# Kernel optimization log

Measured on AMD Instinct MI355X. Metric: run time of the kernel, lower is better.

The kernel has to match this reference:

```python
import math
import jax, jax.numpy as jnp
import numpy as np

H, C, PQ, PV = 8, 256, 8, 12   # no_heads, c_hidden, no_qk_points, no_v_points
INF, EPS = 1e5, 1e-8

def quat_to_rot(q):
    w, x, y, z = q[..., 0], q[..., 1], q[..., 2], q[..., 3]
    r = jnp.stack([
        1 - 2*(y*y + z*z), 2*(x*y - w*z),     2*(x*z + w*y),
        2*(x*y + w*z),     1 - 2*(x*x + z*z), 2*(y*z - w*x),
        2*(x*z - w*y),     2*(y*z + w*x),     1 - 2*(x*x + y*y),
    ], axis=-1)
    return r.reshape(q.shape[:-1] + (3, 3))

def setup_inputs() -> dict:
    key = jax.random.key(0)
    ks = jax.random.split(key, 16)
    B, N, CS, CZ = 1, 512, 384, 128
    s = jax.random.normal(ks[0], (B, N, CS), jnp.float32)
    z = jax.random.normal(ks[1], (B, N, N, CZ), jnp.float32) * 0.1
    quat = jax.random.normal(ks[2], (B, N, 4), jnp.float32)
    quat = quat / jnp.linalg.norm(quat, axis=-1, keepdims=True)
    rot = quat_to_rot(quat)                       # [B,N,3,3] valid rotations
    trans = jax.random.normal(ks[3], (B, N, 3), jnp.float32) * 10.0
    mask = jnp.ones((B, N), jnp.float32)
    g = lambda k, sh: jax.random.normal(k, sh, jnp.float32) * 0.02
    params = dict(
        wq=g(ks[4], (CS, H*C)), bq=jnp.zeros((H*C,), jnp.float32),
        wkv=g(ks[5], (CS, 2*H*C)), bkv=jnp.zeros((2*H*C,), jnp.float32),
        wqp=g(ks[6], (CS, H*PQ*3)), bqp=jnp.zeros((H*PQ*3,), jnp.float32),
        wkvp=g(ks[7], (CS, H*(PQ+PV)*3)), bkvp=jnp.zeros((H*(PQ+PV)*3,), jnp.float32),
        wb=g(ks[8], (CZ, H)), bb=jnp.zeros((H,), jnp.float32),
        wz=g(ks[9], (CZ, CZ//4)), bz=jnp.zeros((CZ//4,), jnp.float32),
        head_weights=jnp.full((H,), 0.541324854612918, jnp.float32),  # softplus^-1(1)
        wo=g(ks[10], (H*(C + 4*PV + CZ//4), CS)), bo=jnp.zeros((CS,), jnp.float32),
    )
    return dict(s=s, z=z, rot=rot, trans=trans, mask=mask, **params)

def reference(s, z, rot, trans, mask, wq, bq, wkv, bkv, wqp, bqp, wkvp, bkvp, wb, bb, wz, bz, head_weights, wo, bo):
    B, N, CS = s.shape
    q = (s @ wq + bq).reshape(B, N, H, C)
    kv = (s @ wkv + bkv).reshape(B, N, H, 2 * C)
    k, v = kv[..., :C], kv[..., C:]

    def split_pts(x):  # torch split-into-3 + stack(-1): [B,N,3*M] -> [B,N,M,3]
        return jnp.moveaxis(x.reshape(B, N, 3, -1), -2, -1)

    def apply_rigid(p):  # global frame: R @ p + t
        return jnp.einsum('bnij,bnpj->bnpi', rot, p) + trans[:, :, None, :]

    q_pts = apply_rigid(split_pts(s @ wqp + bqp)).reshape(B, N, H, PQ, 3)
    kv_pts = apply_rigid(split_pts(s @ wkvp + bkvp)).reshape(B, N, H, PQ + PV, 3)
    k_pts, v_pts = kv_pts[..., :PQ, :], kv_pts[..., PQ:, :]

    b_bias = z @ wb + bb                                  # [B,Ni,Nj,H]
    a = jnp.einsum('bihc,bjhc->bhij', q, k) * math.sqrt(1.0 / (3 * C))
    a = a + math.sqrt(1.0 / 3) * jnp.moveaxis(b_bias, -1, 1)

    disp = q_pts[:, :, None] - k_pts[:, None]             # [B,Ni,Nj,H,PQ,3]
    pt_att = jnp.sum(disp * disp, axis=-1)                # [B,Ni,Nj,H,PQ]
    hw = jax.nn.softplus(head_weights) * math.sqrt(1.0 / (3 * (PQ * 9.0 / 2)))
    pt_att = -0.5 * jnp.sum(pt_att * hw[None, None, None, :, None], axis=-1)  # [B,Ni,Nj,H]

    sq_mask = INF * (mask[:, :, None] * mask[:, None, :] - 1.0)
    a = a + jnp.moveaxis(pt_att, -1, 1) + sq_mask[:, None]
    a = jax.nn.softmax(a, axis=-1)                        # [B,H,Ni,Nj]

    o = jnp.einsum('bhij,bjhc->bihc', a, v).reshape(B, N, H * C)

    o_pt = jnp.einsum('bhij,bjhpd->bihpd', a, v_pts)      # [B,N,H,PV,3] global
    o_pt = jnp.einsum('bnji,bnhpj->bnhpi', rot, o_pt - trans[:, :, None, None, :])  # invert_apply
    o_pt_norm = jnp.sqrt(jnp.sum(o_pt * o_pt, axis=-1) + EPS).reshape(B, N, H * PV)
    o_pt_flat = o_pt.reshape(B, N, H * PV, 3)

    pair_z = z @ wz + bz                                  # [B,Ni,Nj,CZ//4]
    o_pair = jnp.einsum('bhij,bijd->bihd', a, pair_z).reshape(B, N, -1)

    feats = jnp.concatenate(
        [o, o_pt_flat[..., 0], o_pt_flat[..., 1], o_pt_flat[..., 2], o_pt_norm, o_pair], axis=-1)
    return feats @ wo + bo
```

## Files before the change

kernel.cpp:

```cpp
#include <hip/hip_runtime.h>


#define OFF_QBH    0
#define OFF_KBH    524288
#define OFF_VB     1048576
#define OFF_QPRAW  2097152
#define OFF_KVPRAW 2195456
#define OFF_BBIAS  2785280
#define OFF_PAIRZT 3833856
#define OFF_ATTNH  8028160
#define OFF_FEATSB 9076736
#define OFF_WCAT   9764864
#define OFF_WTALL  9767936
#define OFF_VPT    11082752
#define OFF_WOT    11803648
#define OFF_QPTH   12319744
#define OFF_QPTL   12385280
#define OFF_KPTH   12450816
#define OFF_KPTL   12516352
#define OFF_QP2    12581888
#define OFF_KP2    12585984
#define OFF_SBF    12590080

typedef __attribute__((ext_vector_type(8))) short short8;
typedef __attribute__((ext_vector_type(4))) float f32x4;

__device__ __forceinline__ unsigned short f2bf(float f) {
  union { float f; unsigned u; } v; v.f = f;
  unsigned u = v.u;
  unsigned r = (u + 0x7fffu + ((u >> 16) & 1u)) >> 16;
  return (unsigned short)r;
}
__device__ __forceinline__ float bf2f(unsigned short h) {
  union { unsigned u; float f; } v; v.u = ((unsigned)h) << 16; return v.f;
}
__device__ __forceinline__ short8 pack8(float4 a, float4 b) {
  short8 r;
  r[0] = (short)f2bf(a.x); r[1] = (short)f2bf(a.y);
  r[2] = (short)f2bf(a.z); r[3] = (short)f2bf(a.w);
  r[4] = (short)f2bf(b.x); r[5] = (short)f2bf(b.y);
  r[6] = (short)f2bf(b.z); r[7] = (short)f2bf(b.w);
  return r;
}

__global__ __launch_bounds__(256) void prep_all(
    const float* __restrict__ wq, const float* __restrict__ wkv,
    const float* __restrict__ wqp, const float* __restrict__ wkvp,
    const float* __restrict__ wo, const float* __restrict__ wb,
    const float* __restrict__ wz, const float* __restrict__ s,
    unsigned short* __restrict__ wTall, unsigned short* __restrict__ woT,
    unsigned short* __restrict__ wT, unsigned short* __restrict__ sbf) {
  __shared__ float tile[64][65];
  const int b = blockIdx.x, t = threadIdx.x;
  if (b < 642) {
    const int ntile = b % 107, kt = b / 107;
    const float* src; int Nsrc, nloc0;
    const int ng0 = ntile * 64;
    if (ntile < 32)      { src = wq;   Nsrc = 2048; nloc0 = ng0; }
    else if (ntile < 96) { src = wkv;  Nsrc = 4096; nloc0 = ng0 - 2048; }
    else if (ntile < 99) { src = wqp;  Nsrc = 192;  nloc0 = ng0 - 6144; }
    else                 { src = wkvp; Nsrc = 480;  nloc0 = ng0 - 6336; }
    const int r = t >> 2, cs = (t & 3) * 16;
#pragma unroll
    for (int i = 0; i < 16; i += 4) {
      int n = nloc0 + cs + i;
      float4 v;
      if (n + 3 < Nsrc) v = *(const float4*)(src + (size_t)(kt * 64 + r) * Nsrc + n);
      else {
        v.x = (n + 0 < Nsrc) ? src[(size_t)(kt * 64 + r) * Nsrc + n + 0] : 0.f;
        v.y = (n + 1 < Nsrc) ? src[(size_t)(kt * 64 + r) * Nsrc + n + 1] : 0.f;
        v.z = (n + 2 < Nsrc) ? src[(size_t)(kt * 64 + r) * Nsrc + n + 2] : 0.f;
        v.w = (n + 3 < Nsrc) ? src[(size_t)(kt * 64 + r) * Nsrc + n + 3] : 0.f;
      }
      tile[r][cs + i + 0] = v.x; tile[r][cs + i + 1] = v.y;
      tile[r][cs + i + 2] = v.z; tile[r][cs + i + 3] = v.w;
    }
    __syncthreads();
    const int nr = t >> 2, ks = (t & 3) * 16;
    unsigned short ov[16];
#pragma unroll
    for (int i = 0; i < 16; i++) ov[i] = f2bf(tile[ks + i][nr]);
    unsigned short* dst = wTall + (size_t)(ng0 + nr) * 384 + kt * 64 + ks;
    *(uint4*)(dst) = *(const uint4*)&ov[0];
    *(uint4*)(dst + 8) = *(const uint4*)&ov[8];
  } else if (b < 894) {
    const int idx = b - 642;
    const int kt = idx % 42, ntile = idx / 42;
    const int r = t >> 2, cs = (t & 3) * 16;
#pragma unroll
    for (int i = 0; i < 16; i += 4) {
      float4 v = *(const float4*)(wo + (size_t)(kt * 64 + r) * 384 + ntile * 64 + cs + i);
      tile[r][cs + i + 0] = v.x; tile[r][cs + i + 1] = v.y;
      tile[r][cs + i + 2] = v.z; tile[r][cs + i + 3] = v.w;
    }
    __syncthreads();
    const int nr = t >> 2, ks = (t & 3) * 16;
    unsigned short ov[16];
#pragma unroll
    for (int i = 0; i < 16; i++) ov[i] = f2bf(tile[ks + i][nr]);
    unsigned short* dst = woT + (size_t)(ntile * 64 + nr) * 2688 + kt * 64 + ks;
    *(uint4*)(dst) = *(const uint4*)&ov[0];
    *(uint4*)(dst + 8) = *(const uint4*)&ov[8];
  } else if (b < 918) {
    const int l = (b - 894) * 256 + t;
    if (l < 6144) {
      int n = l >> 7, k = l & 127;
      float v = (n < 8) ? wb[k * 8 + n] * 0.5773502691896258f
                        : (n < 40 ? wz[k * 32 + (n - 8)] : 0.f);
      wT[l] = f2bf(v);
    }
  } else {
    const int gid = (b - 918) * 256 + t;
    const int off = gid * 8;
    float4 a0 = *(const float4*)(s + off);
    float4 a1 = *(const float4*)(s + off + 4);
    *(short8*)(sbf + off) = pack8(a0, a1);
  }
}

__global__ __launch_bounds__(256) void mega1(
    const float* __restrict__ z, const unsigned short* __restrict__ wT,
    const float* __restrict__ bb, const float* __restrict__ bz,
    unsigned short* __restrict__ bbias_tb, unsigned short* __restrict__ pairzT,
    const unsigned short* __restrict__ sbf, const unsigned short* __restrict__ wTall,
    const float* __restrict__ bq, const float* __restrict__ bkv,
    const float* __restrict__ bqp, const float* __restrict__ bkvp,
    unsigned short* __restrict__ qbh, unsigned short* __restrict__ kbh,
    float* __restrict__ vb, float* __restrict__ qpraw, float* __restrict__ kvpraw) {
  __shared__ __align__(16) unsigned short lb[4][8][16];
  __shared__ __align__(16) unsigned short lp[4][32][16];
  const int lane = threadIdx.x & 63, wv = threadIdx.x >> 6;
  const int quad = lane >> 4, m = lane & 15;
  if (blockIdx.x < 4096) {
    const int tile = blockIdx.x * 4 + wv;
    const int row0 = tile * 16;
    short8 bf[3][4];
#pragma unroll
    for (int nt = 0; nt < 3; nt++)
#pragma unroll
      for (int s = 0; s < 4; s++)
        bf[nt][s] = *(const short8*)(wT + (size_t)(nt * 16 + m) * 128 + s * 32 + quad * 8);
    float bias[3];
#pragma unroll
    for (int nt = 0; nt < 3; nt++) {
      int c = nt * 16 + m;
      bias[nt] = (c < 8) ? 0.5773502691896258f * bb[c] : (c < 40 ? bz[c - 8] : 0.f);
    }
    f32x4 acc[3];
#pragma unroll
    for (int nt = 0; nt < 3; nt++) acc[nt] = (f32x4){0.f, 0.f, 0.f, 0.f};
    const float* zr = z + (size_t)(row0 + m) * 128 + quad * 8;
#pragma unroll
    for (int s = 0; s < 4; s++) {
      float4 a0 = *(const float4*)(zr + s * 32);
      float4 a1 = *(const float4*)(zr + s * 32 + 4);
      short8 af = pack8(a0, a1);
#pragma unroll
      for (int nt = 0; nt < 3; nt++)
        acc[nt] = __builtin_amdgcn_mfma_f32_16x16x32_bf16(af, bf[nt][s], acc[nt], 0, 0, 0);
    }
#pragma unroll
    for (int nt = 0; nt < 3; nt++) {
      const int c = nt * 16 + m;
#pragma unroll
      for (int r = 0; r < 4; r++) {
        const float v = acc[nt][r] + bias[nt];
        const int jl = quad * 4 + r;
        if (c < 8)       lb[wv][c][jl] = f2bf(v);
        else if (c < 40) lp[wv][c - 8][jl] = f2bf(v);
      }
    }
    const int i = row0 >> 9, j0 = row0 & 511;
    if (lane < 16) {
      int c = lane >> 1, half = lane & 1;
      uint4 val = *(const uint4*)&lb[wv][c][half * 8];
      *(uint4*)(bbias_tb + (size_t)c * 262144 + row0 + half * 8) = val;
    }
    {
      int d = lane >> 1, half = lane & 1;
      uint4 val = *(const uint4*)&lp[wv][d][half * 8];
      *(uint4*)(pairzT + ((size_t)i * 32 + d) * 512 + j0 + half * 8) = val;
    }
  } else {
    const int b2 = blockIdx.x - 4096;
    const int bx = b2 % 107, row0 = (b2 / 107) * 64;
    const int n0 = bx * 64;
    const unsigned short* srow = sbf + (size_t)(row0 + wv * 16 + m) * 384;
    f32x4 acc[4];
#pragma unroll
    for (int nt = 0; nt < 4; nt++) acc[nt] = (f32x4){0.f, 0.f, 0.f, 0.f};
#pragma unroll
    for (int ksx = 0; ksx < 12; ksx++) {
      const int c0 = ksx * 32 + quad * 8;
      short8 af = *(const short8*)(srow + c0);
#pragma unroll
      for (int nt = 0; nt < 4; nt++) {
        short8 bfw = *(const short8*)(wTall + (size_t)(n0 + nt * 16 + m) * 384 + c0);
        acc[nt] = __builtin_amdgcn_mfma_f32_16x16x32_bf16(af, bfw, acc[nt], 0, 0, 0);
      }
    }
    const int rbase = row0 + wv * 16 + quad * 4;
#pragma unroll
    for (int nt = 0; nt < 4; nt++) {
      const int col = n0 + nt * 16 + m;
      if (n0 < 2048) {
        const float bias = bq[col];
#pragma unroll
        for (int r = 0; r < 4; r++)
          qbh[(size_t)(rbase + r) * 2048 + col] = f2bf(acc[nt][r] + bias);
      } else if (n0 < 6144) {
        const int ckv = col - 2048;
        const float bias = bkv[ckv];
        const int hh = ckv >> 9, c = ckv & 511;
        if (c < 256) {
#pragma unroll
          for (int r = 0; r < 4; r++)
            kbh[(size_t)(rbase + r) * 2048 + hh * 256 + c] = f2bf(acc[nt][r] + bias);
        } else {
#pragma unroll
          for (int r = 0; r < 4; r++)
            vb[(size_t)(rbase + r) * 2048 + hh * 256 + (c - 256)] = acc[nt][r] + bias;
        }
      } else if (n0 < 6336) {
        const int cq = col - 6144;
        const float bias = bqp[cq];
#pragma unroll
        for (int r = 0; r < 4; r++)
          qpraw[(size_t)(rbase + r) * 192 + cq] = acc[nt][r] + bias;
      } else {
        const int ck = col - 6336;
        if (ck < 480) {
          const float bias = bkvp[ck];
#pragma unroll
          for (int r = 0; r < 4; r++)
            kvpraw[(size_t)(rbase + r) * 480 + ck] = acc[nt][r] + bias;
        }
      }
    }
  }
}

__global__ __launch_bounds__(256) void mega2(
    const float* __restrict__ vb, const float* __restrict__ qpraw,
    const float* __restrict__ kvpraw, const float* __restrict__ rot,
    const float* __restrict__ trans, unsigned short* __restrict__ vptT,
    unsigned short* __restrict__ qptH, unsigned short* __restrict__ qptL,
    unsigned short* __restrict__ kptH, unsigned short* __restrict__ kptL,
    float* __restrict__ qp2g, float* __restrict__ kp2g) {
  __shared__ float tile[64][65];
  const int b = blockIdx.x, t = threadIdx.x;
  if (b < 320) {
    const int jt = b & 7, h = (b >> 3) & 7, part = b >> 6;
    const int j0 = jt * 64;
    if (part < 4) {
      const int c0 = part * 64;
      const int r = t >> 2, cs = (t & 3) * 16;
#pragma unroll
      for (int ii = 0; ii < 16; ii += 4) {
        float4 v = *(const float4*)(vb + (size_t)(j0 + r) * 2048 + h * 256 + c0 + cs + ii);
        tile[r][cs + ii + 0] = v.x; tile[r][cs + ii + 1] = v.y;
        tile[r][cs + ii + 2] = v.z; tile[r][cs + ii + 3] = v.w;
      }
      __syncthreads();
      const int cl = t >> 2, js = (t & 3) * 16;
      unsigned short ov[16];
#pragma unroll
      for (int x = 0; x < 16; x++) ov[x] = f2bf(tile[js + x][cl]);
      unsigned short* dst = vptT + ((size_t)h * 352 + c0 + cl) * 512 + j0 + js;
      *(uint4*)dst = *(const uint4*)&ov[0];
      *(uint4*)(dst + 8) = *(const uint4*)&ov[8];
    } else {
      float (*lds)[37] = (float(*)[37])&tile[0][0];
      for (int l = t; l < 64 * 36; l += 256) {
        int jl = l / 36, w = l % 36;
        int p = w / 3, d = w % 3;
        const int n = j0 + jl;
        const int pidx = h * 20 + 8 + p;
        const float* kr = kvpraw + (size_t)n * 480;
        float px = kr[pidx], py = kr[160 + pidx], pz = kr[320 + pidx];
        const float* R = rot + n * 9;
        lds[jl][w] = R[d * 3 + 0] * px + R[d * 3 + 1] * py + R[d * 3 + 2] * pz + trans[n * 3 + d];
      }
      __syncthreads();
#pragma unroll
      for (int step = 0; step < 3; step++) {
        int chunk = t + 256 * step;
        int row = chunk >> 3, js = (chunk & 7) * 8;
        unsigned short ov[8];
#pragma unroll
        for (int x = 0; x < 8; x++) {
          int w = (row < 48) ? row : row - 48;
          float f = (w < 36) ? lds[js + x][w] : 0.f;
          unsigned short hi = f2bf(f);
          ov[x] = (row < 48) ? hi : f2bf(f - bf2f(hi));
        }
        *(uint4*)(vptT + ((size_t)h * 352 + 256 + row) * 512 + j0 + js) = *(const uint4*)&ov[0];
      }
    }
  } else {
    const int idx = b - 320;
    const int row = (idx & 1) * 256 + t;
    const int h = idx >> 1;
    const float* R  = rot + row * 9;
    const float* tr = trans + row * 3;
    {
      const float* qr = qpraw + (size_t)row * 192;
      unsigned short hi[32], lo[32]; float s2 = 0.f;
#pragma unroll
      for (int p = 0; p < 8; p++) {
        const int pidx = h * 8 + p;
        float px = qr[pidx], py = qr[64 + pidx], pz = qr[128 + pidx];
        float X = R[0] * px + R[1] * py + R[2] * pz + tr[0];
        float Y = R[3] * px + R[4] * py + R[5] * pz + tr[1];
        float Z = R[6] * px + R[7] * py + R[8] * pz + tr[2];
        hi[p * 3 + 0] = f2bf(X); lo[p * 3 + 0] = f2bf(X - bf2f(hi[p * 3 + 0]));
        hi[p * 3 + 1] = f2bf(Y); lo[p * 3 + 1] = f2bf(Y - bf2f(hi[p * 3 + 1]));
        hi[p * 3 + 2] = f2bf(Z); lo[p * 3 + 2] = f2bf(Z - bf2f(hi[p * 3 + 2]));
        s2 += X * X + Y * Y + Z * Z;
      }
#pragma unroll
      for (int w = 24; w < 32; w++) { hi[w] = 0; lo[w] = 0; }
      unsigned short* dh = qptH + ((size_t)h * 512 + row) * 32;
      unsigned short* dl = qptL + ((size_t)h * 512 + row) * 32;
#pragma unroll
      for (int g = 0; g < 4; g++) {
        *(uint4*)(dh + g * 8) = *(const uint4*)&hi[g * 8];
        *(uint4*)(dl + g * 8) = *(const uint4*)&lo[g * 8];
      }
      qp2g[h * 512 + row] = s2;
    }
    {
      const float* kr = kvpraw + (size_t)row * 480;
      unsigned short hi[32], lo[32]; float s2 = 0.f;
#pragma unroll
      for (int p = 0; p < 8; p++) {
        const int pidx = h * 20 + p;
        float px = kr[pidx], py = kr[160 + pidx], pz = kr[320 + pidx];
        float X = R[0] * px + R[1] * py + R[2] * pz + tr[0];
        float Y = R[3] * px + R[4] * py + R[5] * pz + tr[1];
        float Z = R[6] * px + R[7] * py + R[8] * pz + tr[2];
        hi[p * 3 + 0] = f2bf(X); lo[p * 3 + 0] = f2bf(X - bf2f(hi[p * 3 + 0]));
        hi[p * 3 + 1] = f2bf(Y); lo[p * 3 + 1] = f2bf(Y - bf2f(hi[p * 3 + 1]));
        hi[p * 3 + 2] = f2bf(Z); lo[p * 3 + 2] = f2bf(Z - bf2f(hi[p * 3 + 2]));
        s2 += X * X + Y * Y + Z * Z;
      }
#pragma unroll
      for (int w = 24; w < 32; w++) { hi[w] = 0; lo[w] = 0; }
      unsigned short* dh = kptH + ((size_t)h * 512 + row) * 32;
      unsigned short* dl = kptL + ((size_t)h * 512 + row) * 32;
#pragma unroll
      for (int g = 0; g < 4; g++) {
        *(uint4*)(dh + g * 8) = *(const uint4*)&hi[g * 8];
        *(uint4*)(dl + g * 8) = *(const uint4*)&lo[g * 8];
      }
      kp2g[h * 512 + row] = s2;
    }
  }
}

__global__ __launch_bounds__(512) void logits_fused(
    const unsigned short* __restrict__ qbh, const unsigned short* __restrict__ kbh,
    const unsigned short* __restrict__ qptH, const unsigned short* __restrict__ qptL,
    const unsigned short* __restrict__ kptH, const unsigned short* __restrict__ kptL,
    const float* __restrict__ qp2g, const float* __restrict__ kp2g,
    const unsigned short* __restrict__ bbias_tb, const float* __restrict__ mask,
    const float* __restrict__ hwp, const unsigned short* __restrict__ vptT,
    const float* __restrict__ rot, const float* __restrict__ trans,
    unsigned short* __restrict__ attnh, unsigned short* __restrict__ featsb) {
  const int it = blockIdx.x, h = blockIdx.y;
  const int i0 = it * 16;
  __shared__ __align__(16) unsigned short sth[8][16][72], stl[8][16][72];
  __shared__ float redm[16][8], reds[16][8];
  __shared__ float lds_h[16][48], lds_l[16][48];
  const int t = threadIdx.x;
  const int lane = t & 63, wv = t >> 6;
  const int quad = lane >> 4, m = lane & 15;
  const int jw0 = wv * 64;

  f32x4 acc[4];
#pragma unroll
  for (int nt = 0; nt < 4; nt++) acc[nt] = (f32x4){0.f, 0.f, 0.f, 0.f};
  const unsigned short* qrow = qbh + (size_t)(i0 + m) * 2048 + h * 256;
#pragma unroll
  for (int s = 0; s < 8; s++) {
    short8 af = *(const short8*)(qrow + s * 32 + quad * 8);
#pragma unroll
    for (int nt = 0; nt < 4; nt++) {
      short8 bfr = *(const short8*)(kbh + (size_t)(jw0 + nt * 16 + m) * 2048 + h * 256 + s * 32 + quad * 8);
      acc[nt] = __builtin_amdgcn_mfma_f32_16x16x32_bf16(af, bfr, acc[nt], 0, 0, 0);
    }
  }

  short8 aqh = *(const short8*)(qptH + ((size_t)h * 512 + i0 + m) * 32 + quad * 8);
  short8 aql = *(const short8*)(qptL + ((size_t)h * 512 + i0 + m) * 32 + quad * 8);
  f32x4 accp[4];
#pragma unroll
  for (int nt = 0; nt < 4; nt++) {
    const size_t krow = ((size_t)h * 512 + jw0 + nt * 16 + m) * 32 + quad * 8;
    short8 bkh = *(const short8*)(kptH + krow);
    short8 bkl = *(const short8*)(kptL + krow);
    f32x4 p = (f32x4){0.f, 0.f, 0.f, 0.f};
    p = __builtin_amdgcn_mfma_f32_16x16x32_bf16(aqh, bkh, p, 0, 0, 0);
    p = __builtin_amdgcn_mfma_f32_16x16x32_bf16(aqh, bkl, p, 0, 0, 0);
    p = __builtin_amdgcn_mfma_f32_16x16x32_bf16(aql, bkh, p, 0, 0, 0);
    accp[nt] = p;
  }

  const float c1 = 0.03608439182435161f;
  const float hw = log1pf(expf(hwp[h])) * 0.09622504486493764f;
  float qp2v[4];
#pragma unroll
  for (int r = 0; r < 4; r++) qp2v[r] = qp2g[h * 512 + i0 + quad * 4 + r];
  float lg[4][4];
  float rmax[4] = {-1e30f, -1e30f, -1e30f, -1e30f};
#pragma unroll
  for (int nt = 0; nt < 4; nt++) {
    const int j = jw0 + nt * 16 + m;
    const float kp2v = kp2g[h * 512 + j];
    const float mj = mask[j];
#pragma unroll
    for (int r = 0; r < 4; r++) {
      const int il = quad * 4 + r;
      const float pt = qp2v[r] + kp2v - 2.f * accp[nt][r];
      float v = c1 * acc[nt][r]
              + bf2f(bbias_tb[(size_t)h * 262144 + (size_t)(i0 + il) * 512 + j])
              - 0.5f * hw * pt
              + 100000.f * (mask[i0 + il] * mj - 1.f);
      lg[nt][r] = v;
      rmax[r] = fmaxf(rmax[r], v);
    }
  }
#pragma unroll
  for (int r = 0; r < 4; r++) {
#pragma unroll
    for (int off = 1; off < 16; off <<= 1) rmax[r] = fmaxf(rmax[r], __shfl_xor(rmax[r], off));
  }
  if (m == 0) {
#pragma unroll
    for (int r = 0; r < 4; r++) redm[quad * 4 + r][wv] = rmax[r];
  }
  __syncthreads();
  float rowm[4], rsum[4];
#pragma unroll
  for (int r = 0; r < 4; r++) {
    const int il = quad * 4 + r;
    float m0 = fmaxf(fmaxf(redm[il][0], redm[il][1]), fmaxf(redm[il][2], redm[il][3]));
    float m1 = fmaxf(fmaxf(redm[il][4], redm[il][5]), fmaxf(redm[il][6], redm[il][7]));
    rowm[r] = fmaxf(m0, m1);
    rsum[r] = 0.f;
  }
#pragma unroll
  for (int nt = 0; nt < 4; nt++)
#pragma unroll
    for (int r = 0; r < 4; r++) {
      float e = __expf(lg[nt][r] - rowm[r]);
      lg[nt][r] = e;
      rsum[r] += e;
    }
#pragma unroll
  for (int r = 0; r < 4; r++) {
#pragma unroll
    for (int off = 1; off < 16; off <<= 1) rsum[r] += __shfl_xor(rsum[r], off);
  }
  if (m == 0) {
#pragma unroll
    for (int r = 0; r < 4; r++) reds[quad * 4 + r][wv] = rsum[r];
  }
  __syncthreads();
  float inv[4];
#pragma unroll
  for (int r = 0; r < 4; r++) {
    const int il = quad * 4 + r;
    float s0 = (reds[il][0] + reds[il][1]) + (reds[il][2] + reds[il][3]);
    float s1 = (reds[il][4] + reds[il][5]) + (reds[il][6] + reds[il][7]);
    inv[r] = 1.f / (s0 + s1);
  }
#pragma unroll
  for (int nt = 0; nt < 4; nt++)
#pragma unroll
    for (int r = 0; r < 4; r++) {
      const int il = quad * 4 + r;
      float a = lg[nt][r] * inv[r];
      unsigned short hi = f2bf(a);
      sth[wv][il][nt * 16 + m] = hi;
      stl[wv][il][nt * 16 + m] = f2bf(a - bf2f(hi));
    }
  __syncthreads();
#pragma unroll
  for (int step = 0; step < 2; step++) {
    const int idx = lane + 64 * step;
    const int il = idx >> 3, seg = idx & 7;
    uint4 vh = *(const uint4*)&sth[wv][il][seg * 8];
    *(uint4*)(attnh + ((size_t)h * 512 + i0 + il) * 512 + jw0 + seg * 8) = vh;
  }

  const int nt0 = (wv < 6) ? wv * 3 : 18 + (wv - 6) * 2;
  const int ncnt = (wv < 6) ? 3 : 2;
  f32x4 vacc[3];
#pragma unroll
  for (int k = 0; k < 3; k++) vacc[k] = (f32x4){0.f, 0.f, 0.f, 0.f};
  const unsigned short* vbase = vptT + (size_t)h * 352 * 512;
#pragma unroll
  for (int s = 0; s < 16; s++) {
    const int wsrc = s >> 1, col = (s & 1) * 32 + quad * 8;
    short8 ah = *(const short8*)&sth[wsrc][m][col];
    short8 al = *(const short8*)&stl[wsrc][m][col];
    const int ko = s * 32 + quad * 8;
#pragma unroll
    for (int k = 0; k < 3; k++) {
      if (k < ncnt) {
        const int nt = nt0 + k;
        short8 bfr = *(const short8*)(vbase + (size_t)(nt * 16 + m) * 512 + ko);
        vacc[k] = __builtin_amdgcn_mfma_f32_16x16x32_bf16(ah, bfr, vacc[k], 0, 0, 0);
        if (nt >= 16 && nt < 19)
          vacc[k] = __builtin_amdgcn_mfma_f32_16x16x32_bf16(al, bfr, vacc[k], 0, 0, 0);
      }
    }
  }
#pragma unroll
  for (int k = 0; k < 3; k++) {
    if (k < ncnt) {
      const int nt = nt0 + k;
      if (nt < 16) {
#pragma unroll
        for (int r = 0; r < 4; r++)
          featsb[(size_t)(i0 + quad * 4 + r) * 2688 + h * 256 + nt * 16 + m] = f2bf(vacc[k][r]);
      } else if (nt < 19) {
        const int w = (nt - 16) * 16 + m;
#pragma unroll
        for (int r = 0; r < 4; r++) if (w < 36) lds_h[quad * 4 + r][w] = vacc[k][r];
      } else {
        const int w = (nt - 19) * 16 + m;
#pragma unroll
        for (int r = 0; r < 4; r++) if (w < 36) lds_l[quad * 4 + r][w] = vacc[k][r];
      }
    }
  }
  __syncthreads();
  if (t < 192) {
    const int il = t / 12, p = t % 12, irow = i0 + il;
    const float* R = rot + irow * 9;
    const float* tr = trans + irow * 3;
    float x  = lds_h[il][p * 3 + 0] + lds_l[il][p * 3 + 0] - tr[0];
    float y  = lds_h[il][p * 3 + 1] + lds_l[il][p * 3 + 1] - tr[1];
    float zz = lds_h[il][p * 3 + 2] + lds_l[il][p * 3 + 2] - tr[2];
    float o0 = R[0] * x + R[3] * y + R[6] * zz;
    float o1 = R[1] * x + R[4] * y + R[7] * zz;
    float o2 = R[2] * x + R[5] * y + R[8] * zz;
    float nrm = sqrtf(o0 * o0 + o1 * o1 + o2 * o2 + 1e-8f);
    unsigned short* fr = featsb + (size_t)irow * 2688 + 2048;
    fr[h * 12 + p]       = f2bf(o0);
    fr[96 + h * 12 + p]  = f2bf(o1);
    fr[192 + h * 12 + p] = f2bf(o2);
    fr[288 + h * 12 + p] = f2bf(nrm);
  }
}

__global__ __launch_bounds__(256) void o_pair_mfma(
    const unsigned short* __restrict__ attnh, const unsigned short* __restrict__ pairzT,
    unsigned short* __restrict__ featsb) {
  const int lane = threadIdx.x & 63, wv = threadIdx.x >> 6;
  const int quad = lane >> 4, m = lane & 15;
  const int i = blockIdx.x * 4 + wv;
  f32x4 acc[2];
  acc[0] = (f32x4){0.f, 0.f, 0.f, 0.f};
  acc[1] = (f32x4){0.f, 0.f, 0.f, 0.f};
#pragma unroll
  for (int s = 0; s < 16; s++) {
    const int ko = s * 32 + quad * 8;
    short8 af = *(const short8*)(attnh + (size_t)(m & 7) * 262144 + (size_t)i * 512 + ko);
#pragma unroll
    for (int nt = 0; nt < 2; nt++) {
      short8 bfr = *(const short8*)(pairzT + ((size_t)i * 32 + nt * 16 + m) * 512 + ko);
      acc[nt] = __builtin_amdgcn_mfma_f32_16x16x32_bf16(af, bfr, acc[nt], 0, 0, 0);
    }
  }
  if (quad < 2) {
#pragma unroll
    for (int nt = 0; nt < 2; nt++)
#pragma unroll
      for (int r = 0; r < 4; r++) {
        const int hh = quad * 4 + r, d = nt * 16 + m;
        featsb[(size_t)i * 2688 + 2432 + hh * 32 + d] = f2bf(acc[nt][r]);
      }
  }
}

__global__ __launch_bounds__(256) void out_mfma(
    const unsigned short* __restrict__ featsb, const unsigned short* __restrict__ woT,
    const float* __restrict__ bo, float* __restrict__ out) {
  const int it = blockIdx.x, ng = blockIdx.y;
  const int lane = threadIdx.x & 63, wv = threadIdx.x >> 6;
  const int quad = lane >> 4, m = lane & 15;
  const int i0 = it * 16, n0 = (ng * 4 + wv) * 16;
  const unsigned short* arow = featsb + (size_t)(i0 + m) * 2688;
  const unsigned short* brow = woT + (size_t)(n0 + m) * 2688;
  f32x4 acc = (f32x4){0.f, 0.f, 0.f, 0.f};
#pragma unroll 4
  for (int s = 0; s < 84; s++) {
    const int ko = s * 32 + quad * 8;
    short8 af = *(const short8*)(arow + ko);
    short8 bf = *(const short8*)(brow + ko);
    acc = __builtin_amdgcn_mfma_f32_16x16x32_bf16(af, bf, acc, 0, 0, 0);
  }
  const float bias = bo[n0 + m];
#pragma unroll
  for (int r = 0; r < 4; r++)
    out[(size_t)(i0 + quad * 4 + r) * 384 + n0 + m] = acc[r] + bias;
}

extern "C" void kernel_launch(void* const* d_in, const int* in_sizes, int n_in,
                              void* d_out, int out_size, void* d_ws, size_t ws_size,
                              hipStream_t stream) {
  const float* s     = (const float*)d_in[0];
  const float* z     = (const float*)d_in[1];
  const float* rot   = (const float*)d_in[2];
  const float* trans = (const float*)d_in[3];
  const float* mask  = (const float*)d_in[4];
  const float* wq    = (const float*)d_in[5];
  const float* bq    = (const float*)d_in[6];
  const float* wkv   = (const float*)d_in[7];
  const float* bkv   = (const float*)d_in[8];
  const float* wqp   = (const float*)d_in[9];
  const float* bqp   = (const float*)d_in[10];
  const float* wkvp  = (const float*)d_in[11];
  const float* bkvp  = (const float*)d_in[12];
  const float* wb    = (const float*)d_in[13];
  const float* bb    = (const float*)d_in[14];
  const float* wz    = (const float*)d_in[15];
  const float* bz    = (const float*)d_in[16];
  const float* hwp   = (const float*)d_in[17];
  const float* wo    = (const float*)d_in[18];
  const float* bo    = (const float*)d_in[19];
  float* out = (float*)d_out;

  float* ws = (float*)d_ws;
  unsigned short* qbh   = (unsigned short*)(ws + OFF_QBH);
  unsigned short* kbh   = (unsigned short*)(ws + OFF_KBH);
  float* vb      = ws + OFF_VB;
  float* qpraw   = ws + OFF_QPRAW;
  float* kvpraw  = ws + OFF_KVPRAW;
  unsigned short* bbias_tb = (unsigned short*)(ws + OFF_BBIAS);
  unsigned short* pairzT   = (unsigned short*)(ws + OFF_PAIRZT);
  unsigned short* attnh    = (unsigned short*)(ws + OFF_ATTNH);
  unsigned short* featsb   = (unsigned short*)(ws + OFF_FEATSB);
  unsigned short* wT    = (unsigned short*)(ws + OFF_WCAT);
  unsigned short* wTall = (unsigned short*)(ws + OFF_WTALL);
  unsigned short* vptT  = (unsigned short*)(ws + OFF_VPT);
  unsigned short* woT   = (unsigned short*)(ws + OFF_WOT);
  unsigned short* qptH  = (unsigned short*)(ws + OFF_QPTH);
  unsigned short* qptL  = (unsigned short*)(ws + OFF_QPTL);
  unsigned short* kptH  = (unsigned short*)(ws + OFF_KPTH);
  unsigned short* kptL  = (unsigned short*)(ws + OFF_KPTL);
  float* qp2g = ws + OFF_QP2;
  float* kp2g = ws + OFF_KP2;
  unsigned short* sbf = (unsigned short*)(ws + OFF_SBF);

  prep_all<<<1014, 256, 0, stream>>>(wq, wkv, wqp, wkvp, wo, wb, wz, s,
                                     wTall, woT, wT, sbf);
  mega1<<<4952, 256, 0, stream>>>(z, wT, bb, bz, bbias_tb, pairzT,
                                  sbf, wTall, bq, bkv, bqp, bkvp,
                                  qbh, kbh, vb, qpraw, kvpraw);
  mega2<<<336, 256, 0, stream>>>(vb, qpraw, kvpraw, rot, trans, vptT,
                                 qptH, qptL, kptH, kptL, qp2g, kp2g);
  logits_fused<<<dim3(32, 8), 512, 0, stream>>>(qbh, kbh, qptH, qptL, kptH, kptL,
                                                qp2g, kp2g, bbias_tb, mask, hwp,
                                                vptT, rot, trans, attnh, featsb);
  o_pair_mfma<<<128, 256, 0, stream>>>(attnh, pairzT, featsb);
  out_mfma<<<dim3(32, 6), 256, 0, stream>>>(featsb, woT, bo, out);
}
```

Before: 337.6 us.

## Replace MFMA z-projection with per-thread scalar FP32 FMA using LDS weights

The pair projection (z @ [wb|wz]) in mega1 no longer uses bf16 MFMA tiles with LDS transposes. Each thread now computes one full row of 40 outputs with scalar FP32 FMAs, reading weights converted to float in shared memory, and the grid shrinks from 4096 to 1024 blocks for this part. This removes the z bf16 packing and the LDS staging for transposed stores. In exchange it does far more vector-ALU work, and the strided per-thread reads of z rows are poorly coalesced, which risks lower memory efficiency on a 134MB read.

```diff
diff --git a/kernel.cpp b/kernel.cpp
--- a/kernel.cpp
+++ b/kernel.cpp
@@ -127,62 +127,41 @@
     const float* __restrict__ bqp, const float* __restrict__ bkvp,
     unsigned short* __restrict__ qbh, unsigned short* __restrict__ kbh,
     float* __restrict__ vb, float* __restrict__ qpraw, float* __restrict__ kvpraw) {
-  __shared__ __align__(16) unsigned short lb[4][8][16];
-  __shared__ __align__(16) unsigned short lp[4][32][16];
   const int lane = threadIdx.x & 63, wv = threadIdx.x >> 6;
   const int quad = lane >> 4, m = lane & 15;
-  if (blockIdx.x < 4096) {
-    const int tile = blockIdx.x * 4 + wv;
-    const int row0 = tile * 16;
-    short8 bf[3][4];
-#pragma unroll
-    for (int nt = 0; nt < 3; nt++)
-#pragma unroll
-      for (int s = 0; s < 4; s++)
-        bf[nt][s] = *(const short8*)(wT + (size_t)(nt * 16 + m) * 128 + s * 32 + quad * 8);
-    float bias[3];
-#pragma unroll
-    for (int nt = 0; nt < 3; nt++) {
-      int c = nt * 16 + m;
-      bias[nt] = (c < 8) ? 0.5773502691896258f * bb[c] : (c < 40 ? bz[c - 8] : 0.f);
-    }
-    f32x4 acc[3];
-#pragma unroll
-    for (int nt = 0; nt < 3; nt++) acc[nt] = (f32x4){0.f, 0.f, 0.f, 0.f};
-    const float* zr = z + (size_t)(row0 + m) * 128 + quad * 8;
-#pragma unroll
-    for (int s = 0; s < 4; s++) {
-      float4 a0 = *(const float4*)(zr + s * 32);
-      float4 a1 = *(const float4*)(zr + s * 32 + 4);
-      short8 af = pack8(a0, a1);
-#pragma unroll
-      for (int nt = 0; nt < 3; nt++)
-        acc[nt] = __builtin_amdgcn_mfma_f32_16x16x32_bf16(af, bf[nt][s], acc[nt], 0, 0, 0);
-    }
-#pragma unroll
-    for (int nt = 0; nt < 3; nt++) {
-      const int c = nt * 16 + m;
-#pragma unroll
-      for (int r = 0; r < 4; r++) {
-        const float v = acc[nt][r] + bias[nt];
-        const int jl = quad * 4 + r;
-        if (c < 8)       lb[wv][c][jl] = f2bf(v);
-        else if (c < 40) lp[wv][c - 8][jl] = f2bf(v);
-      }
-    }
-    const int i = row0 >> 9, j0 = row0 & 511;
-    if (lane < 16) {
-      int c = lane >> 1, half = lane & 1;
-      uint4 val = *(const uint4*)&lb[wv][c][half * 8];
-      *(uint4*)(bbias_tb + (size_t)c * 262144 + row0 + half * 8) = val;
-    }
-    {
-      int d = lane >> 1, half = lane & 1;
-      uint4 val = *(const uint4*)&lp[wv][d][half * 8];
-      *(uint4*)(pairzT + ((size_t)i * 32 + d) * 512 + j0 + half * 8) = val;
-    }
+  if (blockIdx.x < 1024) {
+    __shared__ float wTl[40][128];
+    const int t = threadIdx.x;
+    for (int l = t; l < 5120; l += 256)
+      wTl[l >> 7][l & 127] = bf2f(wT[l]);
+    __syncthreads();
+    const int i = blockIdx.x >> 1;
+    const int j = (blockIdx.x & 1) * 256 + t;
+    const int row = i * 512 + j;
+    float acc[40];
+#pragma unroll
+    for (int n = 0; n < 40; n++) acc[n] = 0.f;
+    const float* zr = z + (size_t)row * 128;
+#pragma unroll 4
+    for (int kq = 0; kq < 32; kq++) {
+      float4 zv = *(const float4*)(zr + kq * 4);
+#pragma unroll
+      for (int n = 0; n < 40; n++) {
+        float4 wv4 = *(const float4*)&wTl[n][kq * 4];
+        acc[n] = fmaf(zv.x, wv4.x, acc[n]);
+        acc[n] = fmaf(zv.y, wv4.y, acc[n]);
+        acc[n] = fmaf(zv.z, wv4.z, acc[n]);
+        acc[n] = fmaf(zv.w, wv4.w, acc[n]);
+      }
+    }
+#pragma unroll
+    for (int c = 0; c < 8; c++)
+      bbias_tb[(size_t)c * 262144 + row] = f2bf(acc[c] + 0.5773502691896258f * bb[c]);
+#pragma unroll
+    for (int d = 0; d < 32; d++)
+      pairzT[((size_t)i * 32 + d) * 512 + j] = f2bf(acc[8 + d] + bz[d]);
   } else {
-    const int b2 = blockIdx.x - 4096;
+    const int b2 = blockIdx.x - 1024;
     const int bx = b2 % 107, row0 = (b2 / 107) * 64;
     const int n0 = bx * 64;
     const unsigned short* srow = sbf + (size_t)(row0 + wv * 16 + m) * 384;
@@ -658,7 +637,7 @@
 
   prep_all<<<1014, 256, 0, stream>>>(wq, wkv, wqp, wkvp, wo, wb, wz, s,
                                      wTall, woT, wT, sbf);
-  mega1<<<4952, 256, 0, stream>>>(z, wT, bb, bz, bbias_tb, pairzT,
+  mega1<<<1880, 256, 0, stream>>>(z, wT, bb, bz, bbias_tb, pairzT,
                                   sbf, wTall, bq, bkv, bqp, bkvp,
                                   qbh, kbh, vb, qpraw, kvpraw);
   mega2<<<336, 256, 0, stream>>>(vb, qpraw, kvpraw, rot, trans, vptT,
```

Result: slower. 345.6 us (+2.3%).

## Persist z-projection blocks with double-buffered global-to-LDS loads of z tiles

Applied to the files above, without the earlier changes.

The z projection part of mega1 now runs as 256 persistent blocks, each looping over 16 tiles of 64 rows, instead of 4096 one-shot blocks. Each tile is staged into a double-buffered LDS array through direct global_load_lds, so the next tile's load overlaps the current tile's MFMA work. The weight fragments are loaded once per block rather than once per tile. The cost is 64 KB of LDS per block, which limits occupancy, plus a barrier every iteration, and the prefetch relies on the barrier to make the async LDS writes visible.

```diff
diff --git a/kernel.cpp b/kernel.cpp
--- a/kernel.cpp
+++ b/kernel.cpp
@@ -42,6 +42,11 @@
   r[6] = (short)f2bf(b.z); r[7] = (short)f2bf(b.w);
   return r;
 }
+__device__ __forceinline__ void gl_lds16(const float* g, float* l) {
+  __builtin_amdgcn_global_load_lds(
+      (const __attribute__((address_space(1))) unsigned int*)(g),
+      (__attribute__((address_space(3))) unsigned int*)(l), 16, 0, 0);
+}
 
 __global__ __launch_bounds__(256) void prep_all(
     const float* __restrict__ wq, const float* __restrict__ wkv,
@@ -127,62 +132,85 @@
     const float* __restrict__ bqp, const float* __restrict__ bkvp,
     unsigned short* __restrict__ qbh, unsigned short* __restrict__ kbh,
     float* __restrict__ vb, float* __restrict__ qpraw, float* __restrict__ kvpraw) {
-  __shared__ __align__(16) unsigned short lb[4][8][16];
-  __shared__ __align__(16) unsigned short lp[4][32][16];
   const int lane = threadIdx.x & 63, wv = threadIdx.x >> 6;
   const int quad = lane >> 4, m = lane & 15;
-  if (blockIdx.x < 4096) {
-    const int tile = blockIdx.x * 4 + wv;
-    const int row0 = tile * 16;
-    short8 bf[3][4];
+  if (blockIdx.x < 256) {
+    __shared__ __align__(16) float zt[2][64][128];
+    __shared__ __align__(16) unsigned short lb[4][8][16];
+    __shared__ __align__(16) unsigned short lp[4][32][16];
+    short8 bfw[3][4];
 #pragma unroll
     for (int nt = 0; nt < 3; nt++)
 #pragma unroll
       for (int s = 0; s < 4; s++)
-        bf[nt][s] = *(const short8*)(wT + (size_t)(nt * 16 + m) * 128 + s * 32 + quad * 8);
+        bfw[nt][s] = *(const short8*)(wT + (size_t)(nt * 16 + m) * 128 + s * 32 + quad * 8);
     float bias[3];
 #pragma unroll
     for (int nt = 0; nt < 3; nt++) {
       int c = nt * 16 + m;
       bias[nt] = (c < 8) ? 0.5773502691896258f * bb[c] : (c < 40 ? bz[c - 8] : 0.f);
     }
-    f32x4 acc[3];
-#pragma unroll
-    for (int nt = 0; nt < 3; nt++) acc[nt] = (f32x4){0.f, 0.f, 0.f, 0.f};
-    const float* zr = z + (size_t)(row0 + m) * 128 + quad * 8;
-#pragma unroll
-    for (int s = 0; s < 4; s++) {
-      float4 a0 = *(const float4*)(zr + s * 32);
-      float4 a1 = *(const float4*)(zr + s * 32 + 4);
-      short8 af = pack8(a0, a1);
-#pragma unroll
-      for (int nt = 0; nt < 3; nt++)
-        acc[nt] = __builtin_amdgcn_mfma_f32_16x16x32_bf16(af, bf[nt][s], acc[nt], 0, 0, 0);
-    }
-#pragma unroll
-    for (int nt = 0; nt < 3; nt++) {
-      const int c = nt * 16 + m;
-#pragma unroll
-      for (int r = 0; r < 4; r++) {
-        const float v = acc[nt][r] + bias[nt];
-        const int jl = quad * 4 + r;
-        if (c < 8)       lb[wv][c][jl] = f2bf(v);
-        else if (c < 40) lp[wv][c - 8][jl] = f2bf(v);
-      }
-    }
-    const int i = row0 >> 9, j0 = row0 & 511;
-    if (lane < 16) {
-      int c = lane >> 1, half = lane & 1;
-      uint4 val = *(const uint4*)&lb[wv][c][half * 8];
-      *(uint4*)(bbias_tb + (size_t)c * 262144 + row0 + half * 8) = val;
-    }
+    const int lrow = lane >> 5, lcol = (lane & 31) * 4;
     {
-      int d = lane >> 1, half = lane & 1;
-      uint4 val = *(const uint4*)&lp[wv][d][half * 8];
-      *(uint4*)(pairzT + ((size_t)i * 32 + d) * 512 + j0 + half * 8) = val;
+      const int Tg0 = blockIdx.x * 16;
+#pragma unroll
+      for (int i2 = 0; i2 < 8; i2++) {
+        const int k = wv * 8 + i2;
+        gl_lds16(z + (size_t)(Tg0 * 64 + 2 * k + lrow) * 128 + lcol, &zt[0][2 * k][0]);
+      }
+    }
+    __syncthreads();
+    for (int T = 0; T < 16; T++) {
+      const int buf = T & 1;
+      const int Tg = blockIdx.x * 16 + T;
+      if (T < 15) {
+#pragma unroll
+        for (int i2 = 0; i2 < 8; i2++) {
+          const int k = wv * 8 + i2;
+          gl_lds16(z + (size_t)((Tg + 1) * 64 + 2 * k + lrow) * 128 + lcol,
+                   &zt[buf ^ 1][2 * k][0]);
+        }
+      }
+      f32x4 acc[3];
+#pragma unroll
+      for (int nt = 0; nt < 3; nt++) acc[nt] = (f32x4){0.f, 0.f, 0.f, 0.f};
+#pragma unroll
+      for (int s = 0; s < 4; s++) {
+        const float* zr = &zt[buf][wv * 16 + m][s * 32 + quad * 8];
+        float4 a0 = *(const float4*)(zr);
+        float4 a1 = *(const float4*)(zr + 4);
+        short8 af = pack8(a0, a1);
+#pragma unroll
+        for (int nt = 0; nt < 3; nt++)
+          acc[nt] = __builtin_amdgcn_mfma_f32_16x16x32_bf16(af, bfw[nt][s], acc[nt], 0, 0, 0);
+      }
+#pragma unroll
+      for (int nt = 0; nt < 3; nt++) {
+        const int c = nt * 16 + m;
+#pragma unroll
+        for (int r = 0; r < 4; r++) {
+          const float v = acc[nt][r] + bias[nt];
+          const int jl = quad * 4 + r;
+          if (c < 8)       lb[wv][c][jl] = f2bf(v);
+          else if (c < 40) lp[wv][c - 8][jl] = f2bf(v);
+        }
+      }
+      const int row0 = Tg * 64 + wv * 16;
+      const int i = row0 >> 9, j0 = row0 & 511;
+      if (lane < 16) {
+        int c = lane >> 1, half = lane & 1;
+        uint4 val = *(const uint4*)&lb[wv][c][half * 8];
+        *(uint4*)(bbias_tb + (size_t)c * 262144 + row0 + half * 8) = val;
+      }
+      {
+        int d = lane >> 1, half = lane & 1;
+        uint4 val = *(const uint4*)&lp[wv][d][half * 8];
+        *(uint4*)(pairzT + ((size_t)i * 32 + d) * 512 + j0 + half * 8) = val;
+      }
+      __syncthreads();
     }
   } else {
-    const int b2 = blockIdx.x - 4096;
+    const int b2 = blockIdx.x - 256;
     const int bx = b2 % 107, row0 = (b2 / 107) * 64;
     const int n0 = bx * 64;
     const unsigned short* srow = sbf + (size_t)(row0 + wv * 16 + m) * 384;
@@ -195,8 +223,8 @@
       short8 af = *(const short8*)(srow + c0);
 #pragma unroll
       for (int nt = 0; nt < 4; nt++) {
-        short8 bfw = *(const short8*)(wTall + (size_t)(n0 + nt * 16 + m) * 384 + c0);
-        acc[nt] = __builtin_amdgcn_mfma_f32_16x16x32_bf16(af, bfw, acc[nt], 0, 0, 0);
+        short8 bfw2 = *(const short8*)(wTall + (size_t)(n0 + nt * 16 + m) * 384 + c0);
+        acc[nt] = __builtin_amdgcn_mfma_f32_16x16x32_bf16(af, bfw2, acc[nt], 0, 0, 0);
       }
     }
     const int rbase = row0 + wv * 16 + quad * 4;
@@ -658,7 +686,7 @@
 
   prep_all<<<1014, 256, 0, stream>>>(wq, wkv, wqp, wkvp, wo, wb, wz, s,
                                      wTall, woT, wT, sbf);
-  mega1<<<4952, 256, 0, stream>>>(z, wT, bb, bz, bbias_tb, pairzT,
+  mega1<<<1112, 256, 0, stream>>>(z, wT, bb, bz, bbias_tb, pairzT,
                                   sbf, wTall, bq, bkv, bqp, bkvp,
                                   qbh, kbh, vb, qpraw, kvpraw);
   mega2<<<336, 256, 0, stream>>>(vb, qpraw, kvpraw, rot, trans, vptT,
```

Result: faster. 323.2 us (-4.3%).
